# Performance work log

Hardware: AMD Instinct MI355X
Metric: run time of the kernel (lower is better)

## Reference

```python
import jax, jax.numpy as jnp
import numpy as np

N = 4096
D = 1024  # hidden_size == att_size


def setup_inputs() -> dict:
    key = jax.random.key(0)
    ks = jax.random.split(key, 10)
    s = 0.02
    return {
        "q": jax.random.normal(ks[0], (N, D), jnp.float32),
        "k": jax.random.normal(ks[1], (N, D), jnp.float32),
        "v": jax.random.normal(ks[2], (N, D), jnp.float32),
        "bias": jax.random.normal(ks[3], (N, N), jnp.float32) * s,
        "Wq": jax.random.normal(ks[4], (D, D), jnp.float32) * s,
        "bq": jnp.zeros((D,), jnp.float32),
        "Wk": jax.random.normal(ks[5], (D, D), jnp.float32) * s,
        "bk": jnp.zeros((D,), jnp.float32),
        "Wv": jax.random.normal(ks[6], (D, D), jnp.float32) * s,
        "bv": jnp.zeros((D,), jnp.float32),
    }


def reference(q, k, v, bias, Wq, bq, Wk, bk, Wv, bv):
    d = q.shape[-1]
    scale = d ** (-0.5)
    # QKV projections (nn.Linear: x @ W.T + b)
    qp = (q @ Wq.T + bq) * scale          # [N, D]
    kp = k @ Wk.T + bk                    # [N, D]
    vp = v @ Wv.T + bv                    # [N, D]
    # full N x N attention (single head, pseudo-batch of 1 in the original)
    scores = qp @ kp.T                    # [N, N]
    att = jax.nn.softmax(scores, axis=-1) + bias  # POST-softmax bias add
    # dropout is identity in eval mode; original casts weights to fp32 here
    out = att.astype(jnp.float32) @ vp    # [N, D]
    return out
```

## Files before the change

### kernel.cpp

```cpp
#include <hip/hip_runtime.h>
#include <hip/hip_bf16.h>
#include <stdint.h>

typedef unsigned short u16;
using bf16x8 = __attribute__((ext_vector_type(8))) __bf16;
using f32x4  = __attribute__((ext_vector_type(4))) float;

__device__ __forceinline__ u16 f2bf(float f) {
    union { float f; unsigned u; } a; a.f = f;
    unsigned u = a.u;
    u += 0x7fffu + ((u >> 16) & 1u);
    return (u16)(u >> 16);
}

__device__ __forceinline__ void gload_lds16(const void* g, void* l) {
    __builtin_amdgcn_global_load_lds(
        (const __attribute__((address_space(1))) void*)g,
        (__attribute__((address_space(3))) void*)l, 16, 0, 0);
}

__device__ __forceinline__ void gemm_core(const u16* __restrict__ A,
                                          const u16* __restrict__ B,
                                          int K, int bm, int bn,
                                          u16* sA, u16* sB,
                                          f32x4 acc[4][4])
{
    const int tid  = threadIdx.x;
    const int lane = tid & 63;
    const int wm   = (tid >> 7) & 1;
    const int wn   = (tid >> 6) & 1;

    const u16* Ag0 = A + (long)(bm * 128 + (tid >> 2)) * K + (tid & 3) * 8;
    const u16* Ag1 = Ag0 + (long)64 * K;
    const u16* Bg0 = B + (long)(bn * 128 + (tid >> 2)) * K + (tid & 3) * 8;
    const u16* Bg1 = Bg0 + (long)64 * K;
    u16* la0 = sA + tid * 8;
    u16* la1 = sA + 2048 + tid * 8;
    u16* lb0 = sB + tid * 8;
    u16* lb1 = sB + 2048 + tid * 8;

    const u16* ra = sA + (wm * 64 + (lane & 15)) * 32 + (lane >> 4) * 8;
    const u16* rb = sB + (wn * 64 + (lane & 15)) * 32 + (lane >> 4) * 8;

    for (int k0 = 0; k0 < K; k0 += 32) {
        gload_lds16(Ag0 + k0, la0);
        gload_lds16(Ag1 + k0, la1);
        gload_lds16(Bg0 + k0, lb0);
        gload_lds16(Bg1 + k0, lb1);
        __syncthreads();
        bf16x8 af[4], bfr[4];
#pragma unroll
        for (int i = 0; i < 4; i++) af[i]  = *(const bf16x8*)(ra + i * 512);
#pragma unroll
        for (int i = 0; i < 4; i++) bfr[i] = *(const bf16x8*)(rb + i * 512);
#pragma unroll
        for (int mi = 0; mi < 4; mi++)
#pragma unroll
            for (int ni = 0; ni < 4; ni++)
                acc[mi][ni] = __builtin_amdgcn_mfma_f32_16x16x32_bf16(
                    af[mi], bfr[ni], acc[mi][ni], 0, 0, 0);
        __syncthreads();
    }
}

__global__ __launch_bounds__(256)
void cast6(const float* __restrict__ q, const float* __restrict__ k,
           const float* __restrict__ v, const float* __restrict__ wq,
           const float* __restrict__ wk, const float* __restrict__ wv,
           u16* __restrict__ qb, u16* __restrict__ kb, u16* __restrict__ vb,
           u16* __restrict__ wqb, u16* __restrict__ wkb, u16* __restrict__ wvb,
           int nqkv, int nw)
{
    const int z = blockIdx.y;
    const float* s; u16* d; int n;
    switch (z) {
        case 0:  s = q;  d = qb;  n = nqkv; break;
        case 1:  s = k;  d = kb;  n = nqkv; break;
        case 2:  s = v;  d = vb;  n = nqkv; break;
        case 3:  s = wq; d = wqb; n = nw;   break;
        case 4:  s = wk; d = wkb; n = nw;   break;
        default: s = wv; d = wvb; n = nw;   break;
    }
    long i = ((long)blockIdx.x * 256 + threadIdx.x) * 8;
    if (i >= n) return;
    float4 a = *(const float4*)(s + i);
    float4 b = *(const float4*)(s + i + 4);
    ushort4 o0, o1;
    o0.x = f2bf(a.x); o0.y = f2bf(a.y); o0.z = f2bf(a.z); o0.w = f2bf(a.w);
    o1.x = f2bf(b.x); o1.y = f2bf(b.y); o1.z = f2bf(b.z); o1.w = f2bf(b.w);
    *(ushort4*)(d + i)     = o0;
    *(ushort4*)(d + i + 4) = o1;
}

__global__ __launch_bounds__(256, 2)
void proj_gemm(const u16* __restrict__ qb, const u16* __restrict__ kb,
               const u16* __restrict__ vb, const u16* __restrict__ wqb,
               const u16* __restrict__ wkb, const u16* __restrict__ wvb,
               const float* __restrict__ bq, const float* __restrict__ bk,
               const float* __restrict__ bv,
               u16* __restrict__ qp, u16* __restrict__ kp, u16* __restrict__ vpT)
{
    __shared__ __align__(16) u16 sA[4096];
    __shared__ __align__(16) u16 sB[4096];
    const int z = blockIdx.z;
    const u16* A = (z == 0) ? qb : (z == 1) ? kb : vb;
    const u16* B = (z == 0) ? wqb : (z == 1) ? wkb : wvb;
    const float* bias = (z == 0) ? bq : (z == 1) ? bk : bv;
    u16* OUT = (z == 0) ? qp : (z == 1) ? kp : vpT;
    const float scale = (z == 0) ? 0.03125f : 1.0f;

    f32x4 acc[4][4] = {};
    gemm_core(A, B, 1024, blockIdx.y, blockIdx.x, sA, sB, acc);

    const int lane = threadIdx.x & 63;
    const int wm   = (threadIdx.x >> 7) & 1;
    const int wn   = (threadIdx.x >> 6) & 1;
    const int m0 = blockIdx.y * 128 + wm * 64 + ((lane >> 4) << 2);
    const int n0 = blockIdx.x * 128 + wn * 64 + (lane & 15);
#pragma unroll
    for (int mi = 0; mi < 4; mi++)
#pragma unroll
        for (int ni = 0; ni < 4; ni++) {
            const int gm = m0 + mi * 16;
            const int gn = n0 + ni * 16;
            const float bb = bias[gn];
#pragma unroll
            for (int r = 0; r < 4; r++) {
                float val = (acc[mi][ni][r] + bb) * scale;
                if (z < 2) OUT[(long)(gm + r) * 1024 + gn] = f2bf(val);
                else       OUT[(long)gn * 4096 + gm + r]   = f2bf(val);
            }
        }
}

__global__ __launch_bounds__(256, 2)
void score_gemm(const u16* __restrict__ qp, const u16* __restrict__ kp,
                float* __restrict__ S)
{
    __shared__ __align__(16) u16 sA[4096];
    __shared__ __align__(16) u16 sB[4096];
    f32x4 acc[4][4] = {};
    gemm_core(qp, kp, 1024, blockIdx.y, blockIdx.x, sA, sB, acc);

    const int lane = threadIdx.x & 63;
    const int wm   = (threadIdx.x >> 7) & 1;
    const int wn   = (threadIdx.x >> 6) & 1;
    const int m0 = blockIdx.y * 128 + wm * 64 + ((lane >> 4) << 2);
    const int n0 = blockIdx.x * 128 + wn * 64 + (lane & 15);
#pragma unroll
    for (int mi = 0; mi < 4; mi++)
#pragma unroll
        for (int ni = 0; ni < 4; ni++) {
            const int gm = m0 + mi * 16;
            const int gn = n0 + ni * 16;
#pragma unroll
            for (int r = 0; r < 4; r++)
                S[(long)(gm + r) * 4096 + gn] = acc[mi][ni][r];
        }
}

__global__ __launch_bounds__(256)
void softmax_bias(const float* __restrict__ S, const float* __restrict__ bias,
                  u16* __restrict__ att)
{
    const long row = blockIdx.x;
    const int tid = threadIdx.x;
    const float4* srow = (const float4*)(S + row * 4096);
    float4 v[4];
    float mx = -3.0e38f;
#pragma unroll
    for (int i = 0; i < 4; i++) {
        v[i] = srow[tid + i * 256];
        mx = fmaxf(mx, fmaxf(fmaxf(v[i].x, v[i].y), fmaxf(v[i].z, v[i].w)));
    }
#pragma unroll
    for (int o = 32; o >= 1; o >>= 1) mx = fmaxf(mx, __shfl_xor(mx, o, 64));
    __shared__ float red[8];
    if ((tid & 63) == 0) red[tid >> 6] = mx;
    __syncthreads();
    mx = fmaxf(fmaxf(red[0], red[1]), fmaxf(red[2], red[3]));
    float sum = 0.f;
#pragma unroll
    for (int i = 0; i < 4; i++) {
        v[i].x = __expf(v[i].x - mx); v[i].y = __expf(v[i].y - mx);
        v[i].z = __expf(v[i].z - mx); v[i].w = __expf(v[i].w - mx);
        sum += (v[i].x + v[i].y) + (v[i].z + v[i].w);
    }
#pragma unroll
    for (int o = 32; o >= 1; o >>= 1) sum += __shfl_xor(sum, o, 64);
    if ((tid & 63) == 0) red[4 + (tid >> 6)] = sum;
    __syncthreads();
    const float inv = 1.0f / (red[4] + red[5] + red[6] + red[7]);

    const float4* brow = (const float4*)(bias + row * 4096);
    ushort4* arow = (ushort4*)(att + row * 4096);
#pragma unroll
    for (int i = 0; i < 4; i++) {
        float4 b = brow[tid + i * 256];
        ushort4 o4;
        o4.x = f2bf(v[i].x * inv + b.x);
        o4.y = f2bf(v[i].y * inv + b.y);
        o4.z = f2bf(v[i].z * inv + b.z);
        o4.w = f2bf(v[i].w * inv + b.w);
        arow[tid + i * 256] = o4;
    }
}

__global__ __launch_bounds__(256, 2)
void out_gemm(const u16* __restrict__ att, const u16* __restrict__ vpT,
              float* __restrict__ O)
{
    __shared__ __align__(16) u16 sA[4096];
    __shared__ __align__(16) u16 sB[4096];
    f32x4 acc[4][4] = {};
    gemm_core(att, vpT, 4096, blockIdx.y, blockIdx.x, sA, sB, acc);

    const int lane = threadIdx.x & 63;
    const int wm   = (threadIdx.x >> 7) & 1;
    const int wn   = (threadIdx.x >> 6) & 1;
    const int m0 = blockIdx.y * 128 + wm * 64 + ((lane >> 4) << 2);
    const int n0 = blockIdx.x * 128 + wn * 64 + (lane & 15);
#pragma unroll
    for (int mi = 0; mi < 4; mi++)
#pragma unroll
        for (int ni = 0; ni < 4; ni++) {
            const int gm = m0 + mi * 16;
            const int gn = n0 + ni * 16;
#pragma unroll
            for (int r = 0; r < 4; r++)
                O[(long)(gm + r) * 1024 + gn] = acc[mi][ni][r];
        }
}

extern "C" void kernel_launch(void* const* d_in, const int* in_sizes, int n_in,
                              void* d_out, int out_size, void* d_ws, size_t ws_size,
                              hipStream_t stream)
{
    const float* q    = (const float*)d_in[0];
    const float* k    = (const float*)d_in[1];
    const float* v    = (const float*)d_in[2];
    const float* bias = (const float*)d_in[3];
    const float* Wq   = (const float*)d_in[4];
    const float* bq   = (const float*)d_in[5];
    const float* Wk   = (const float*)d_in[6];
    const float* bk   = (const float*)d_in[7];
    const float* Wv   = (const float*)d_in[8];
    const float* bv   = (const float*)d_in[9];
    float* out = (float*)d_out;

    uint8_t* ws = (uint8_t*)d_ws;
    const size_t MB = 1u << 20;
    u16* qb  = (u16*)(ws);
    u16* kb  = (u16*)(ws + 8 * MB);
    u16* vb  = (u16*)(ws + 16 * MB);
    u16* wqb = (u16*)(ws + 24 * MB);
    u16* wkb = (u16*)(ws + 26 * MB);
    u16* wvb = (u16*)(ws + 28 * MB);
    u16* qp  = (u16*)(ws + 30 * MB);
    u16* kp  = (u16*)(ws + 38 * MB);
    u16* vpT = (u16*)(ws + 46 * MB);
    float* S = (float*)(ws + 54 * MB);
    u16* att = (u16*)(ws);

    cast6<<<dim3(2048, 6), 256, 0, stream>>>(q, k, v, Wq, Wk, Wv,
                                             qb, kb, vb, wqb, wkb, wvb,
                                             4096 * 1024, 1024 * 1024);
    proj_gemm<<<dim3(8, 32, 3), 256, 0, stream>>>(qb, kb, vb, wqb, wkb, wvb,
                                                  bq, bk, bv, qp, kp, vpT);
    score_gemm<<<dim3(32, 32), 256, 0, stream>>>(qp, kp, S);
    softmax_bias<<<dim3(4096), 256, 0, stream>>>(S, bias, att);
    out_gemm<<<dim3(8, 32), 256, 0, stream>>>(att, vpT, out);
}
```

Measured before the change: 332.9 us.

## Store scores in bf16 and split-K the output GEMM with partial-sum reduction

```diff
diff --git a/kernel.cpp b/kernel.cpp
--- a/kernel.cpp
+++ b/kernel.cpp
@@ -12,6 +12,9 @@
     u += 0x7fffu + ((u >> 16) & 1u);
     return (u16)(u >> 16);
 }
+__device__ __forceinline__ float bf2f(unsigned bits_hi16) {
+    union { unsigned u; float f; } a; a.u = bits_hi16; return a.f;
+}
 
 __device__ __forceinline__ void gload_lds16(const void* g, void* l) {
     __builtin_amdgcn_global_load_lds(
@@ -21,7 +24,8 @@
 
 __device__ __forceinline__ void gemm_core(const u16* __restrict__ A,
                                           const u16* __restrict__ B,
-                                          int K, int bm, int bn,
+                                          int lda, int ldb, int kLen,
+                                          int bm, int bn,
                                           u16* sA, u16* sB,
                                           f32x4 acc[4][4])
 {
@@ -30,10 +34,10 @@
     const int wm   = (tid >> 7) & 1;
     const int wn   = (tid >> 6) & 1;
 
-    const u16* Ag0 = A + (long)(bm * 128 + (tid >> 2)) * K + (tid & 3) * 8;
-    const u16* Ag1 = Ag0 + (long)64 * K;
-    const u16* Bg0 = B + (long)(bn * 128 + (tid >> 2)) * K + (tid & 3) * 8;
-    const u16* Bg1 = Bg0 + (long)64 * K;
+    const u16* Ag0 = A + (long)(bm * 128 + (tid >> 2)) * lda + (tid & 3) * 8;
+    const u16* Ag1 = Ag0 + (long)64 * lda;
+    const u16* Bg0 = B + (long)(bn * 128 + (tid >> 2)) * ldb + (tid & 3) * 8;
+    const u16* Bg1 = Bg0 + (long)64 * ldb;
     u16* la0 = sA + tid * 8;
     u16* la1 = sA + 2048 + tid * 8;
     u16* lb0 = sB + tid * 8;
@@ -42,7 +46,7 @@
     const u16* ra = sA + (wm * 64 + (lane & 15)) * 32 + (lane >> 4) * 8;
     const u16* rb = sB + (wn * 64 + (lane & 15)) * 32 + (lane >> 4) * 8;
 
-    for (int k0 = 0; k0 < K; k0 += 32) {
+    for (int k0 = 0; k0 < kLen; k0 += 32) {
         gload_lds16(Ag0 + k0, la0);
         gload_lds16(Ag1 + k0, la1);
         gload_lds16(Bg0 + k0, lb0);
@@ -110,7 +114,7 @@
     const float scale = (z == 0) ? 0.03125f : 1.0f;
 
     f32x4 acc[4][4] = {};
-    gemm_core(A, B, 1024, blockIdx.y, blockIdx.x, sA, sB, acc);
+    gemm_core(A, B, 1024, 1024, 1024, blockIdx.y, blockIdx.x, sA, sB, acc);
 
     const int lane = threadIdx.x & 63;
     const int wm   = (threadIdx.x >> 7) & 1;
@@ -135,12 +139,12 @@
 
 __global__ __launch_bounds__(256, 2)
 void score_gemm(const u16* __restrict__ qp, const u16* __restrict__ kp,
-                float* __restrict__ S)
+                u16* __restrict__ S)
 {
     __shared__ __align__(16) u16 sA[4096];
     __shared__ __align__(16) u16 sB[4096];
     f32x4 acc[4][4] = {};
-    gemm_core(qp, kp, 1024, blockIdx.y, blockIdx.x, sA, sB, acc);
+    gemm_core(qp, kp, 1024, 1024, 1024, blockIdx.y, blockIdx.x, sA, sB, acc);
 
     const int lane = threadIdx.x & 63;
     const int wm   = (threadIdx.x >> 7) & 1;
@@ -155,24 +159,32 @@
             const int gn = n0 + ni * 16;
 #pragma unroll
             for (int r = 0; r < 4; r++)
-                S[(long)(gm + r) * 4096 + gn] = acc[mi][ni][r];
+                S[(long)(gm + r) * 4096 + gn] = f2bf(acc[mi][ni][r]);
         }
 }
 
 __global__ __launch_bounds__(256)
-void softmax_bias(const float* __restrict__ S, const float* __restrict__ bias,
+void softmax_bias(const u16* __restrict__ S, const float* __restrict__ bias,
                   u16* __restrict__ att)
 {
     const long row = blockIdx.x;
     const int tid = threadIdx.x;
-    const float4* srow = (const float4*)(S + row * 4096);
-    float4 v[4];
-    float mx = -3.0e38f;
-#pragma unroll
-    for (int i = 0; i < 4; i++) {
-        v[i] = srow[tid + i * 256];
-        mx = fmaxf(mx, fmaxf(fmaxf(v[i].x, v[i].y), fmaxf(v[i].z, v[i].w)));
+    const u16* srow = S + row * 4096 + tid * 16;
+
+    float v[16];
+    {
+        uint4 a = *(const uint4*)(srow);
+        uint4 b = *(const uint4*)(srow + 8);
+        unsigned w[8] = {a.x, a.y, a.z, a.w, b.x, b.y, b.z, b.w};
+#pragma unroll
+        for (int i = 0; i < 8; i++) {
+            v[2 * i]     = bf2f(w[i] << 16);
+            v[2 * i + 1] = bf2f(w[i] & 0xffff0000u);
+        }
     }
+    float mx = v[0];
+#pragma unroll
+    for (int i = 1; i < 16; i++) mx = fmaxf(mx, v[i]);
 #pragma unroll
     for (int o = 32; o >= 1; o >>= 1) mx = fmaxf(mx, __shfl_xor(mx, o, 64));
     __shared__ float red[8];
@@ -181,39 +193,43 @@
     mx = fmaxf(fmaxf(red[0], red[1]), fmaxf(red[2], red[3]));
     float sum = 0.f;
 #pragma unroll
-    for (int i = 0; i < 4; i++) {
-        v[i].x = __expf(v[i].x - mx); v[i].y = __expf(v[i].y - mx);
-        v[i].z = __expf(v[i].z - mx); v[i].w = __expf(v[i].w - mx);
-        sum += (v[i].x + v[i].y) + (v[i].z + v[i].w);
-    }
+    for (int i = 0; i < 16; i++) { v[i] = __expf(v[i] - mx); sum += v[i]; }
 #pragma unroll
     for (int o = 32; o >= 1; o >>= 1) sum += __shfl_xor(sum, o, 64);
     if ((tid & 63) == 0) red[4 + (tid >> 6)] = sum;
     __syncthreads();
     const float inv = 1.0f / (red[4] + red[5] + red[6] + red[7]);
 
-    const float4* brow = (const float4*)(bias + row * 4096);
-    ushort4* arow = (ushort4*)(att + row * 4096);
+    const float4* brow = (const float4*)(bias + row * 4096 + tid * 16);
+    unsigned o[8];
 #pragma unroll
     for (int i = 0; i < 4; i++) {
-        float4 b = brow[tid + i * 256];
-        ushort4 o4;
-        o4.x = f2bf(v[i].x * inv + b.x);
-        o4.y = f2bf(v[i].y * inv + b.y);
-        o4.z = f2bf(v[i].z * inv + b.z);
-        o4.w = f2bf(v[i].w * inv + b.w);
-        arow[tid + i * 256] = o4;
+        float4 b = brow[i];
+        unsigned lo = f2bf(v[4 * i + 0] * inv + b.x);
+        unsigned hi = f2bf(v[4 * i + 1] * inv + b.y);
+        o[2 * i] = lo | (hi << 16);
+        lo = f2bf(v[4 * i + 2] * inv + b.z);
+        hi = f2bf(v[4 * i + 3] * inv + b.w);
+        o[2 * i + 1] = lo | (hi << 16);
     }
+    u16* arow = att + row * 4096 + tid * 16;
+    *(uint4*)(arow)     = make_uint4(o[0], o[1], o[2], o[3]);
+    *(uint4*)(arow + 8) = make_uint4(o[4], o[5], o[6], o[7]);
 }
 
 __global__ __launch_bounds__(256, 2)
 void out_gemm(const u16* __restrict__ att, const u16* __restrict__ vpT,
-              float* __restrict__ O)
+              float* __restrict__ P)
 {
     __shared__ __align__(16) u16 sA[4096];
     __shared__ __align__(16) u16 sB[4096];
+    const int z = blockIdx.z;
+    const u16* A = att + z * 2048;
+    const u16* B = vpT + z * 2048;
+    float* O = P + (long)z * 4096 * 1024;
+
     f32x4 acc[4][4] = {};
-    gemm_core(att, vpT, 4096, blockIdx.y, blockIdx.x, sA, sB, acc);
+    gemm_core(A, B, 4096, 4096, 2048, blockIdx.y, blockIdx.x, sA, sB, acc);
 
     const int lane = threadIdx.x & 63;
     const int wm   = (threadIdx.x >> 7) & 1;
@@ -230,6 +246,17 @@
             for (int r = 0; r < 4; r++)
                 O[(long)(gm + r) * 1024 + gn] = acc[mi][ni][r];
         }
+}
+
+__global__ __launch_bounds__(256)
+void addp(const float* __restrict__ P, float* __restrict__ O)
+{
+    long i = ((long)blockIdx.x * 256 + threadIdx.x) * 4;
+    float4 a = *(const float4*)(P + i);
+    float4 b = *(const float4*)(P + 4194304 + i);
+    float4 r;
+    r.x = a.x + b.x; r.y = a.y + b.y; r.z = a.z + b.z; r.w = a.w + b.w;
+    *(float4*)(O + i) = r;
 }
 
 extern "C" void kernel_launch(void* const* d_in, const int* in_sizes, int n_in,
@@ -259,8 +286,9 @@
     u16* qp  = (u16*)(ws + 30 * MB);
     u16* kp  = (u16*)(ws + 38 * MB);
     u16* vpT = (u16*)(ws + 46 * MB);
-    float* S = (float*)(ws + 54 * MB);
+    u16* S   = (u16*)(ws + 54 * MB);
     u16* att = (u16*)(ws);
+    float* P = (float*)(ws + 86 * MB);
 
     cast6<<<dim3(2048, 6), 256, 0, stream>>>(q, k, v, Wq, Wk, Wv,
                                              qb, kb, vb, wqb, wkb, wvb,
@@ -269,5 +297,6 @@
                                                   bq, bk, bv, qp, kp, vpT);
     score_gemm<<<dim3(32, 32), 256, 0, stream>>>(qp, kp, S);
     softmax_bias<<<dim3(4096), 256, 0, stream>>>(S, bias, att);
-    out_gemm<<<dim3(8, 32), 256, 0, stream>>>(att, vpT, out);
-}
+    out_gemm<<<dim3(8, 32, 2), 256, 0, stream>>>(att, vpT, P);
+    addp<<<dim3(4096), 256, 0, stream>>>(P, out);
+}
```

Measured after the change: 313.2 us. 5.9% less time.
